# Optimization experiments

Hardware: AMD Instinct MI355X
Metric: run time of the kernel (lower is better)

The kernel has to match this reference:

```python
import jax, jax.numpy as jnp
import numpy as np

BATCH, H_IMG, W_IMG = 4, 256, 512
HIDDEN, LAYERS, IN_CH = 64, 3, 3


def grid_edges(h, w):
    # torch_geometric.utils.grid: 8-connected grid + self-loops (9-point stencil).
    idx = np.arange(h * w, dtype=np.int32).reshape(h, w)
    srcs, dsts = [], []
    for dy in (-1, 0, 1):
        for dx in (-1, 0, 1):
            dst = idx[max(0, -dy):h - max(0, dy), max(0, -dx):w - max(0, dx)]
            src = idx[max(0, dy):h + min(0, dy), max(0, dx):w + min(0, dx)]
            srcs.append(src.ravel())
            dsts.append(dst.ravel())
    return np.concatenate(srcs), np.concatenate(dsts)


def setup_inputs() -> dict:
    key = jax.random.key(0)
    ks = jax.random.split(key, 8)
    src_np, dst_np = grid_edges(H_IMG, W_IMG)
    s = 0.1
    return {
        "x": jax.random.normal(ks[0], (BATCH, IN_CH, H_IMG, W_IMG), jnp.float32),
        "src": jnp.asarray(src_np, jnp.int32),
        "dst": jnp.asarray(dst_np, jnp.int32),
        "W_in": jax.random.normal(ks[1], (IN_CH, HIDDEN), jnp.float32) * s,
        "b_in": jnp.zeros((HIDDEN,), jnp.float32),
        "Wg": jax.random.normal(ks[2], (LAYERS, HIDDEN, HIDDEN), jnp.float32) * s,
        "bg": jnp.zeros((LAYERS, HIDDEN), jnp.float32),
        "W_out": jax.random.normal(ks[3], (HIDDEN, IN_CH), jnp.float32) * s,
        "b_out": jnp.zeros((IN_CH,), jnp.float32),
    }


def reference(x, src, dst, W_in, b_in, Wg, bg, W_out, b_out):
    B, C, H, W = x.shape
    N = H * W
    # [B,C,H,W] -> [B,N,C]
    xn = x.reshape(B, C, N).transpose(0, 2, 1)
    h = xn @ W_in + b_in
    # GCN symmetric normalization (all edge weights 1; self-loops already present)
    deg = jax.ops.segment_sum(jnp.ones(src.shape[0], x.dtype), dst, num_segments=N)
    dinv = jax.lax.rsqrt(jnp.maximum(deg, 1e-12))
    norm = dinv[src] * dinv[dst]  # [E]

    def aggregate(m):  # m: [E, HIDDEN] -> [N, HIDDEN]
        return jax.ops.segment_sum(m, dst, num_segments=N)

    for l in range(Wg.shape[0]):
        hl = h @ Wg[l]                              # [B,N,hd]
        msg = norm[None, :, None] * hl[:, src, :]   # gather + scale: [B,E,hd]
        agg = jax.vmap(aggregate)(msg)              # scatter-add:   [B,N,hd]
        h = jax.nn.relu(agg + bg[l])                # dropout inactive (eval mode)

    out = h @ W_out + b_out                         # [B,N,3]
    return out.transpose(0, 2, 1).reshape(B, C, H, W)
```

## Files before the change

### kernel.cpp

```cpp
#include <hip/hip_runtime.h>
#include <hip/hip_fp16.h>

#define H_IMG 256
#define W_IMG 512
#define NPIX  (H_IMG*W_IMG)
#define BATCH 4
#define HID   64

#define TX 32
#define TY 8
#define HX (TX+2)
#define HY (TY+2)
#define HN (HX*HY)
#define LTH 256


typedef _Float16 half8 __attribute__((ext_vector_type(8)));
typedef float v4f __attribute__((ext_vector_type(4)));

#define GLOAD16(gp, lp) \
  __builtin_amdgcn_global_load_lds((const __attribute__((address_space(1))) unsigned int*)(gp), \
                                   (__attribute__((address_space(3))) unsigned int*)(lp), 16, 0, 0)

__device__ __forceinline__ float rs1(int v, int n) {
  return rsqrtf((float)(3 - (v==0) - (v==(n-1))));
}
__device__ __forceinline__ float dinvf(int y, int x) {
  int cy = 3 - (y==0) - (y==(H_IMG-1));
  int cx = 3 - (x==0) - (x==(W_IMG-1));
  return rsqrtf((float)(cy*cx));
}

__device__ __forceinline__ unsigned pack2(float a, float b) {
  __half2 h = __floats2half2_rn(a, b);
  return *reinterpret_cast<unsigned*>(&h);
}

__device__ __forceinline__ void fma_mix2(float& accL, float& accH, unsigned hv, float s) {
  asm("v_fma_mix_f32 %0, %2, %3, %0 op_sel:[0,0,0] op_sel_hi:[1,0,0]\n\t"
      "v_fma_mix_f32 %1, %2, %3, %1 op_sel:[1,0,0] op_sel_hi:[1,0,0]"
      : "+v"(accL), "+v"(accH)
      : "v"(hv), "v"(s));
}

__global__ void k_wg(const float* __restrict__ Wg, __half* __restrict__ WgT) {
  int idx = blockIdx.x * 256 + threadIdx.x;
  int l = idx >> 12, rem = idx & 4095;
  int f = rem >> 6, k = rem & 63;
  WgT[idx] = __float2half(Wg[(l << 12) + (k << 6) + f]);
}

__global__ void k_prep2(const __half* __restrict__ src, __half* __restrict__ dst) {
  int idx = blockIdx.x * 256 + threadIdx.x;
  if (idx < 4096) dst[idx] = src[idx];
}

template<int MODE>
__global__ __launch_bounds__(LTH, 3) void k_layer(
    const float* __restrict__ x,
    const float* __restrict__ W_in, const float* __restrict__ b_in,
    const __half* __restrict__ hin, const __half* __restrict__ wgt,
    const float* __restrict__ bg, __half* __restrict__ hout,
    const float* __restrict__ W_out, const float* __restrict__ b_out,
    float* __restrict__ outp) {
  __shared__ __half hs[HN * 64];
  const int tid = threadIdx.x;
  const int tx0 = blockIdx.x * TX;
  const int ty0 = blockIdx.y * TY;
  const int b   = blockIdx.z;

  const int l64 = tid & 63, lm = l64 & 15, lh = l64 >> 4, w = tid >> 6;

  half8 af0[4], af1[4];
  v4f cb[4];
#pragma unroll
  for (int ft = 0; ft < 4; ++ft) {
    const __half* wp = wgt + (ft*16 + lm)*64 + lh*8;
    af0[ft] = *(const half8*)wp;
    af1[ft] = *(const half8*)(wp + 32);
    cb[ft] = *(const v4f*)(bg + ft*16 + (lh << 2));
  }

  if (MODE == 0) {
    const float* xb = x + (size_t)b*3*NPIX;
    for (int n = tid; n < HN; n += LTH) {
      int row = n / HX, col = n - row*HX;
      int gy = ty0 - 1 + row, gx = tx0 - 1 + col;
      __half* hp = &hs[n << 6];
      const int s7 = n & 7;
      if ((unsigned)gy < H_IMG && (unsigned)gx < W_IMG) {
        int gi = (gy << 9) + gx;
        float x0 = xb[gi], x1 = xb[NPIX+gi], x2 = xb[2*NPIX+gi];
#pragma unroll
        for (int c8 = 0; c8 < 8; ++c8) {
          float rr[8];
#pragma unroll
          for (int k = 0; k < 8; ++k) {
            int f = (c8 << 3) + k;
            rr[k] = fmaf(x0, W_in[f], fmaf(x1, W_in[64+f], fmaf(x2, W_in[128+f], b_in[f])));
          }
          uint4 u = make_uint4(pack2(rr[0],rr[1]), pack2(rr[2],rr[3]),
                               pack2(rr[4],rr[5]), pack2(rr[6],rr[7]));
          *(uint4*)(hp + ((c8 ^ s7) << 3)) = u;
        }
      } else {
        uint4 z = make_uint4(0u,0u,0u,0u);
#pragma unroll
        for (int c8 = 0; c8 < 8; ++c8)
          *(uint4*)(hp + ((c8 ^ s7) << 3)) = z;
      }
    }
  } else {
    const __half* hb = hin + (size_t)b * NPIX * HID;
    for (int it = tid; it < HN*8; it += LTH) {
      int nl = it >> 3;
      int c8s = (it & 7) ^ (nl & 7);
      int row = nl / HX, col = nl - row*HX;
      int sy = ty0 - 1 + row, sx = tx0 - 1 + col;
      sy = max(0, min(H_IMG-1, sy));
      sx = max(0, min(W_IMG-1, sx));
      const __half* gp = hb + ((size_t)((sy << 9) + sx)) * 64 + (c8s << 3);
      GLOAD16(gp, &hs[it << 3]);
    }
  }
  __syncthreads();

  if (MODE != 2) {
    __half* ho = hout + (size_t)b * NPIX * HID;
#pragma unroll
    for (int i = 0; i < 4; ++i) {
      const int g  = (w << 2) + i;
      const int nn = (g << 4) + lm;
      const int r = nn >> 5, c = nn & 31;
      const int gy = ty0 + r, gx = tx0 + c;
      float ry[3] = {rs1(gy-1,H_IMG), rs1(gy,H_IMG), rs1(gy+1,H_IMG)};
      float rx[3] = {rs1(gx-1,W_IMG), rs1(gx,W_IMG), rs1(gx+1,W_IMG)};
      const float dcc = ry[1]*rx[1];
      float a0[8] = {0,0,0,0,0,0,0,0};
      float a1[8] = {0,0,0,0,0,0,0,0};
#pragma unroll
      for (int dr = 0; dr < 3; ++dr) {
#pragma unroll
        for (int dx = 0; dx < 3; ++dx) {
          int ny = gy - 1 + dr, nx = gx - 1 + dx;
          bool ok = ((unsigned)ny < H_IMG) && ((unsigned)nx < W_IMG);
          float s = ok ? dcc * ry[dr] * rx[dx] : 0.f;
          int nj = (r + dr)*HX + (c + dx);
          const __half* base = &hs[nj << 6];
          uint4 va = *(const uint4*)(base + ((lh ^ (nj & 7)) << 3));
          uint4 vb = *(const uint4*)(base + (((lh + 4) ^ (nj & 7)) << 3));
          fma_mix2(a0[0], a0[1], va.x, s);
          fma_mix2(a0[2], a0[3], va.y, s);
          fma_mix2(a0[4], a0[5], va.z, s);
          fma_mix2(a0[6], a0[7], va.w, s);
          fma_mix2(a1[0], a1[1], vb.x, s);
          fma_mix2(a1[2], a1[3], vb.y, s);
          fma_mix2(a1[4], a1[5], vb.z, s);
          fma_mix2(a1[6], a1[7], vb.w, s);
        }
      }
      half8 b0, b1;
#pragma unroll
      for (int k = 0; k < 8; ++k) { b0[k] = (_Float16)a0[k]; b1[k] = (_Float16)a1[k]; }
      v4f d[4];
#pragma unroll
      for (int ft = 0; ft < 4; ++ft) {
        v4f t = __builtin_amdgcn_mfma_f32_16x16x32_f16(af0[ft], b0, cb[ft], 0, 0, 0);
        d[ft]  = __builtin_amdgcn_mfma_f32_16x16x32_f16(af1[ft], b1, t,     0, 0, 0);
      }
      __half* hp = ho + (size_t)(((ty0 + r) << 9) + tx0 + c) * HID + (lh << 2);
#pragma unroll
      for (int ft = 0; ft < 4; ++ft) {
        uint2 u;
        u.x = pack2(fmaxf(d[ft][0], 0.f), fmaxf(d[ft][1], 0.f));
        u.y = pack2(fmaxf(d[ft][2], 0.f), fmaxf(d[ft][3], 0.f));
        *(uint2*)(hp + ft*16) = u;
      }
    }
    return;
  }

  {
    const int lx = tid & 31, ly = tid >> 5;
    const int gy = ty0 + ly, gx = tx0 + lx;
    const float dc = dinvf(gy, gx);
    float sc[9];
    int   nbn[9];
#pragma unroll
    for (int r = 0; r < 3; ++r)
#pragma unroll
      for (int c = 0; c < 3; ++c) {
        int ny = gy - 1 + r, nx = gx - 1 + c;
        bool ok = ((unsigned)ny < H_IMG) && ((unsigned)nx < W_IMG);
        sc[r*3+c] = ok ? dc * dinvf(ny, nx) : 0.f;
        nbn[r*3+c] = (ly + r)*HX + lx + c;
      }
    half8 sreg[8];
#pragma unroll
    for (int ch = 0; ch < 8; ++ch) {
      float acc[8] = {0.f,0.f,0.f,0.f,0.f,0.f,0.f,0.f};
#pragma unroll
      for (int j = 0; j < 9; ++j) {
        int nj = nbn[j];
        uint4 v = *(const uint4*)&hs[(nj << 6) + (((ch ^ (nj & 7))) << 3)];
        float s = sc[j];
        fma_mix2(acc[0], acc[1], v.x, s);
        fma_mix2(acc[2], acc[3], v.y, s);
        fma_mix2(acc[4], acc[5], v.z, s);
        fma_mix2(acc[6], acc[7], v.w, s);
      }
      half8 o;
#pragma unroll
      for (int k = 0; k < 8; ++k) o[k] = (_Float16)acc[k];
      sreg[ch] = o;
    }
    __syncthreads();

    {
      __half* hp = &hs[tid << 6];
      const int s7 = tid & 7;
#pragma unroll
      for (int ch = 0; ch < 8; ++ch)
        *(half8*)(hp + ((ch ^ s7) << 3)) = sreg[ch];
    }
    __syncthreads();

#pragma unroll
    for (int i = 0; i < 4; ++i) {
      int g  = (w << 2) + i;
      int nn = (g << 4) + lm;
      const int s7 = nn & 7;
      const __half* np = &hs[nn << 6];
      half8 b0 = *(const half8*)(np + ((lh ^ s7) << 3));
      half8 b1 = *(const half8*)(np + (((lh + 4) ^ s7) << 3));
      v4f d[4];
#pragma unroll
      for (int ft = 0; ft < 4; ++ft) {
        v4f t = __builtin_amdgcn_mfma_f32_16x16x32_f16(af0[ft], b0, cb[ft], 0, 0, 0);
        d[ft]  = __builtin_amdgcn_mfma_f32_16x16x32_f16(af1[ft], b1, t,     0, 0, 0);
      }
      __half* hp = &hs[nn << 6];
#pragma unroll
      for (int ft = 0; ft < 4; ++ft) {
        int pos = ft*16 + (lh << 2);
        int c8 = pos >> 3, sub = pos & 7;
        uint2 u;
        u.x = pack2(fmaxf(d[ft][0], 0.f), fmaxf(d[ft][1], 0.f));
        u.y = pack2(fmaxf(d[ft][2], 0.f), fmaxf(d[ft][3], 0.f));
        *(uint2*)(hp + ((c8 ^ s7) << 3) + sub) = u;
      }
    }

    __syncthreads();
    const int prow = tid >> 5, pcol = tid & 31;
    const int pgi = ((ty0 + prow) << 9) + tx0 + pcol;
    const __half* hp = &hs[tid << 6];
    const int s7p = tid & 7;
    float p0 = b_out[0], p1 = b_out[1], p2 = b_out[2];
#pragma unroll
    for (int o = 0; o < 8; ++o) {
      half8 v = *(const half8*)(hp + ((o ^ s7p) << 3));
#pragma unroll
      for (int e = 0; e < 8; ++e) {
        const float* wr = W_out + (o*8 + e)*3;
        float fv = (float)v[e];
        p0 = fmaf(fv, wr[0], p0);
        p1 = fmaf(fv, wr[1], p1);
        p2 = fmaf(fv, wr[2], p2);
      }
    }
    float* ob = outp + (size_t)b*3*NPIX;
    ob[pgi] = p0; ob[NPIX + pgi] = p1; ob[2*NPIX + pgi] = p2;
  }
}

extern "C" void kernel_launch(void* const* d_in, const int* in_sizes, int n_in,
                              void* d_out, int out_size, void* d_ws, size_t ws_size,
                              hipStream_t stream) {
  const float* x     = (const float*)d_in[0];
  const float* W_in  = (const float*)d_in[3];
  const float* b_in  = (const float*)d_in[4];
  const float* Wg    = (const float*)d_in[5];
  const float* bg    = (const float*)d_in[6];
  const float* W_out = (const float*)d_in[7];
  const float* b_out = (const float*)d_in[8];
  float* out = (float*)d_out;

  __half* WgT = (__half*)d_out;
  __half* hA = (__half*)d_ws;
  __half* hB = hA + (size_t)BATCH*NPIX*HID;
  __half* w2c = hA;

  k_wg<<<dim3(48), 256, 0, stream>>>(Wg, WgT);

  dim3 lg(W_IMG/TX, H_IMG/TY, BATCH);
  k_layer<0><<<lg, LTH, 0, stream>>>(x, W_in, b_in, nullptr, WgT, bg, hA,
                                     nullptr, nullptr, nullptr);
  k_layer<1><<<lg, LTH, 0, stream>>>(nullptr, nullptr, nullptr, hA, WgT + 4096, bg + 64, hB,
                                     nullptr, nullptr, nullptr);
  k_prep2<<<dim3(16), 256, 0, stream>>>(WgT + 8192, w2c);
  k_layer<2><<<lg, LTH, 0, stream>>>(nullptr, nullptr, nullptr, hB, w2c, bg + 128, nullptr,
                                     W_out, b_out, out);
}
```

Before: 104.2 us.

## Split halo load into two phases and unify final-layer path with MFMA aggregation

Halo staging is split: the first six halo rows are loaded and synchronized, then the remaining rows are issued while the first half of the output rows (which only need rows 0-5) are aggregated. The final layer (MODE 2) now reuses the same per-wave register aggregation plus MFMA path instead of a separate per-thread stencil, LDS round trip and second MFMA pass, then stages the results in LDS for the output projection. This removes an LDS write/read and a barrier for the last layer, and overlaps global loads with compute, at the cost of more live registers for buffered outputs.

```diff
diff --git a/kernel.cpp b/kernel.cpp
--- a/kernel.cpp
+++ b/kernel.cpp
@@ -12,6 +12,7 @@
 #define HX (TX+2)
 #define HY (TY+2)
 #define HN (HX*HY)
+#define NA (6*HX)
 #define LTH 256
 
 
@@ -24,11 +25,6 @@
 
 __device__ __forceinline__ float rs1(int v, int n) {
   return rsqrtf((float)(3 - (v==0) - (v==(n-1))));
-}
-__device__ __forceinline__ float dinvf(int y, int x) {
-  int cy = 3 - (y==0) - (y==(H_IMG-1));
-  int cx = 3 - (x==0) - (x==(W_IMG-1));
-  return rsqrtf((float)(cy*cx));
 }
 
 __device__ __forceinline__ unsigned pack2(float a, float b) {
@@ -81,9 +77,11 @@
     cb[ft] = *(const v4f*)(bg + ft*16 + (lh << 2));
   }
 
-  if (MODE == 0) {
-    const float* xb = x + (size_t)b*3*NPIX;
-    for (int n = tid; n < HN; n += LTH) {
+  const float* xb = (MODE == 0) ? (x + (size_t)b*3*NPIX) : nullptr;
+  const __half* hb = (MODE != 0) ? (hin + (size_t)b * NPIX * HID) : nullptr;
+
+  auto stage0 = [&](int nlo, int nhi) {
+    for (int n = nlo + tid; n < nhi; n += LTH) {
       int row = n / HX, col = n - row*HX;
       int gy = ty0 - 1 + row, gx = tx0 - 1 + col;
       __half* hp = &hs[n << 6];
@@ -110,9 +108,9 @@
           *(uint4*)(hp + ((c8 ^ s7) << 3)) = z;
       }
     }
-  } else {
-    const __half* hb = hin + (size_t)b * NPIX * HID;
-    for (int it = tid; it < HN*8; it += LTH) {
+  };
+  auto stage1 = [&](int itlo, int ithi) {
+    for (int it = itlo + tid; it < ithi; it += LTH) {
       int nl = it >> 3;
       int c8s = (it & 7) ^ (nl & 7);
       int row = nl / HX, col = nl - row*HX;
@@ -122,14 +120,19 @@
       const __half* gp = hb + ((size_t)((sy << 9) + sx)) * 64 + (c8s << 3);
       GLOAD16(gp, &hs[it << 3]);
     }
-  }
+  };
+
+  if (MODE == 0) stage0(0, NA); else stage1(0, NA*8);
   __syncthreads();
-
-  if (MODE != 2) {
-    __half* ho = hout + (size_t)b * NPIX * HID;
-#pragma unroll
-    for (int i = 0; i < 4; ++i) {
-      const int g  = (w << 2) + i;
+  if (MODE == 0) stage0(NA, HN); else stage1(NA*8, HN*8);
+
+  __half* ho = (MODE != 2) ? (hout + (size_t)b * NPIX * HID) : nullptr;
+  uint2 uo[2][2][4];
+#pragma unroll
+  for (int ph = 0; ph < 2; ++ph) {
+#pragma unroll
+    for (int i = 0; i < 2; ++i) {
+      const int g  = (ph << 3) + (w << 1) + i;
       const int nn = (g << 4) + lm;
       const int r = nn >> 5, c = nn & 31;
       const int gy = ty0 + r, gx = tx0 + c;
@@ -168,89 +171,43 @@
         v4f t = __builtin_amdgcn_mfma_f32_16x16x32_f16(af0[ft], b0, cb[ft], 0, 0, 0);
         d[ft]  = __builtin_amdgcn_mfma_f32_16x16x32_f16(af1[ft], b1, t,     0, 0, 0);
       }
-      __half* hp = ho + (size_t)(((ty0 + r) << 9) + tx0 + c) * HID + (lh << 2);
-#pragma unroll
-      for (int ft = 0; ft < 4; ++ft) {
-        uint2 u;
-        u.x = pack2(fmaxf(d[ft][0], 0.f), fmaxf(d[ft][1], 0.f));
-        u.y = pack2(fmaxf(d[ft][2], 0.f), fmaxf(d[ft][3], 0.f));
-        *(uint2*)(hp + ft*16) = u;
-      }
-    }
-    return;
+      if (MODE != 2) {
+        __half* hp = ho + (size_t)(((ty0 + r) << 9) + tx0 + c) * HID + (lh << 2);
+#pragma unroll
+        for (int ft = 0; ft < 4; ++ft) {
+          uint2 u;
+          u.x = pack2(fmaxf(d[ft][0], 0.f), fmaxf(d[ft][1], 0.f));
+          u.y = pack2(fmaxf(d[ft][2], 0.f), fmaxf(d[ft][3], 0.f));
+          *(uint2*)(hp + ft*16) = u;
+        }
+      } else {
+#pragma unroll
+        for (int ft = 0; ft < 4; ++ft) {
+          uo[ph][i][ft].x = pack2(fmaxf(d[ft][0], 0.f), fmaxf(d[ft][1], 0.f));
+          uo[ph][i][ft].y = pack2(fmaxf(d[ft][2], 0.f), fmaxf(d[ft][3], 0.f));
+        }
+      }
+    }
+    if (ph == 0) __syncthreads();
   }
 
-  {
-    const int lx = tid & 31, ly = tid >> 5;
-    const int gy = ty0 + ly, gx = tx0 + lx;
-    const float dc = dinvf(gy, gx);
-    float sc[9];
-    int   nbn[9];
-#pragma unroll
-    for (int r = 0; r < 3; ++r)
-#pragma unroll
-      for (int c = 0; c < 3; ++c) {
-        int ny = gy - 1 + r, nx = gx - 1 + c;
-        bool ok = ((unsigned)ny < H_IMG) && ((unsigned)nx < W_IMG);
-        sc[r*3+c] = ok ? dc * dinvf(ny, nx) : 0.f;
-        nbn[r*3+c] = (ly + r)*HX + lx + c;
-      }
-    half8 sreg[8];
-#pragma unroll
-    for (int ch = 0; ch < 8; ++ch) {
-      float acc[8] = {0.f,0.f,0.f,0.f,0.f,0.f,0.f,0.f};
-#pragma unroll
-      for (int j = 0; j < 9; ++j) {
-        int nj = nbn[j];
-        uint4 v = *(const uint4*)&hs[(nj << 6) + (((ch ^ (nj & 7))) << 3)];
-        float s = sc[j];
-        fma_mix2(acc[0], acc[1], v.x, s);
-        fma_mix2(acc[2], acc[3], v.y, s);
-        fma_mix2(acc[4], acc[5], v.z, s);
-        fma_mix2(acc[6], acc[7], v.w, s);
-      }
-      half8 o;
-#pragma unroll
-      for (int k = 0; k < 8; ++k) o[k] = (_Float16)acc[k];
-      sreg[ch] = o;
-    }
+  if (MODE == 2) {
     __syncthreads();
-
-    {
-      __half* hp = &hs[tid << 6];
-      const int s7 = tid & 7;
-#pragma unroll
-      for (int ch = 0; ch < 8; ++ch)
-        *(half8*)(hp + ((ch ^ s7) << 3)) = sreg[ch];
-    }
-    __syncthreads();
-
-#pragma unroll
-    for (int i = 0; i < 4; ++i) {
-      int g  = (w << 2) + i;
-      int nn = (g << 4) + lm;
-      const int s7 = nn & 7;
-      const __half* np = &hs[nn << 6];
-      half8 b0 = *(const half8*)(np + ((lh ^ s7) << 3));
-      half8 b1 = *(const half8*)(np + (((lh + 4) ^ s7) << 3));
-      v4f d[4];
-#pragma unroll
-      for (int ft = 0; ft < 4; ++ft) {
-        v4f t = __builtin_amdgcn_mfma_f32_16x16x32_f16(af0[ft], b0, cb[ft], 0, 0, 0);
-        d[ft]  = __builtin_amdgcn_mfma_f32_16x16x32_f16(af1[ft], b1, t,     0, 0, 0);
-      }
-      __half* hp = &hs[nn << 6];
-#pragma unroll
-      for (int ft = 0; ft < 4; ++ft) {
-        int pos = ft*16 + (lh << 2);
-        int c8 = pos >> 3, sub = pos & 7;
-        uint2 u;
-        u.x = pack2(fmaxf(d[ft][0], 0.f), fmaxf(d[ft][1], 0.f));
-        u.y = pack2(fmaxf(d[ft][2], 0.f), fmaxf(d[ft][3], 0.f));
-        *(uint2*)(hp + ((c8 ^ s7) << 3) + sub) = u;
-      }
-    }
-
+#pragma unroll
+    for (int ph = 0; ph < 2; ++ph)
+#pragma unroll
+      for (int i = 0; i < 2; ++i) {
+        const int g  = (ph << 3) + (w << 1) + i;
+        const int nn = (g << 4) + lm;
+        const int s7 = nn & 7;
+        __half* hp = &hs[nn << 6];
+#pragma unroll
+        for (int ft = 0; ft < 4; ++ft) {
+          int pos = ft*16 + (lh << 2);
+          int c8 = pos >> 3, sub = pos & 7;
+          *(uint2*)(hp + ((c8 ^ s7) << 3) + sub) = uo[ph][i][ft];
+        }
+      }
     __syncthreads();
     const int prow = tid >> 5, pcol = tid & 31;
     const int pgi = ((ty0 + prow) << 9) + tx0 + pcol;
```

Measured after the change: 109.1 us. 1.05x slower.
